# Kernel tuning notes

Hardware: AMD Instinct MI355X
Metric: run time of the kernel (lower is better)

The kernel has to match this reference:

```python
import jax, jax.numpy as jnp
import numpy as np

B, T = 64, 20          # batch, caption length
C, HW = 512, 196       # cnn_channels, width*height (14x14)
V, E, U = 10000, 256, 512  # n_tokens, emb_size, lstm_units
MAX_NORM = 5.0


def setup_inputs() -> dict:
    key = jax.random.key(0)
    ks = jax.random.split(key, 12)
    s = 0.02
    return {
        "image_features": jax.random.normal(ks[0], (B, C, HW), jnp.float32),
        "captions_ix": jax.random.randint(ks[1], (B, T), 0, V, dtype=jnp.int32),
        "W_h0": jax.random.normal(ks[2], (U, C), jnp.float32) * s,
        "b_h0": jnp.zeros((U,), jnp.float32),
        "W_c0": jax.random.normal(ks[3], (U, C), jnp.float32) * s,
        "b_c0": jnp.zeros((U,), jnp.float32),
        "emb": jax.random.normal(ks[4], (V, E), jnp.float32) * s,
        "W_key": jax.random.normal(ks[5], (U, C), jnp.float32) * s,
        "b_key": jnp.zeros((U,), jnp.float32),
        "W_ih": jax.random.normal(ks[6], (4 * U, C + E), jnp.float32) * s,
        "b_ih": jnp.zeros((4 * U,), jnp.float32),
        "W_hh": jax.random.normal(ks[7], (4 * U, U), jnp.float32) * s,
        "b_hh": jnp.zeros((4 * U,), jnp.float32),
        "W_out": jax.random.normal(ks[8], (V, C + E + U), jnp.float32) * s,
        "b_out": jnp.zeros((V,), jnp.float32),
    }


def _caption_net(image_features, captions_ix, W_h0, b_h0, W_c0, b_c0, emb,
                 W_key, b_key, W_ih, b_ih, W_hh, b_hh, W_out, b_out):
    feats_mean = image_features.mean(axis=2)                # [B, C]
    hid0 = feats_mean @ W_h0.T + b_h0                       # [B, U]
    cell0 = feats_mean @ W_c0.T + b_c0                      # [B, U]
    feats = jnp.transpose(image_features, (0, 2, 1))        # [B, HW, C]
    keys = feats @ W_key.T + b_key                          # [B, HW, U]

    # nn.Embedding(max_norm=5): renorm rows whose L2 norm exceeds 5
    norms = jnp.linalg.norm(emb, axis=1, keepdims=True)
    emb_eff = emb * jnp.minimum(1.0, MAX_NORM / jnp.maximum(norms, 1e-12))
    cap_emb = emb_eff[captions_ix]                          # [B, T, E]

    inv_scale = 1.0 / (keys.shape[2] ** 0.5)

    def step(carry, emb_t):
        hid, cell = carry
        # scaled dot-product attention, query = current hidden state
        scores = jnp.einsum('bu,bku->bk', hid, keys) * inv_scale   # [B, HW]
        w = jax.nn.softmax(scores, axis=1)
        a = jnp.einsum('bk,bkc->bc', w, feats)                     # [B, C]
        x = jnp.concatenate([emb_t, a], axis=1)                    # [B, E+C]
        gates = x @ W_ih.T + b_ih + hid @ W_hh.T + b_hh            # [B, 4U]
        i, f, g, o = jnp.split(gates, 4, axis=1)
        cell = jax.nn.sigmoid(f) * cell + jax.nn.sigmoid(i) * jnp.tanh(g)
        hid = jax.nn.sigmoid(o) * jnp.tanh(cell)
        out = jnp.concatenate([hid, a, emb_t], axis=1)             # [B, U+C+E]
        return (hid, cell), (out, w)

    (_, _), (outs, attn) = jax.lax.scan(step, (hid0, cell0),
                                        jnp.transpose(cap_emb, (1, 0, 2)))
    outs = jnp.transpose(outs, (1, 0, 2))                   # [B, T, U+C+E]
    attn = jnp.transpose(attn, (1, 0, 2))                   # [B, T, HW]
    logits = outs @ W_out.T + b_out                         # [B, T, V]
    return logits, attn


def reference(image_features, captions_ix, W_h0, b_h0, W_c0, b_c0, emb,
              W_key, b_key, W_ih, b_ih, W_hh, b_hh, W_out, b_out):
    return _caption_net(image_features, captions_ix, W_h0, b_h0, W_c0, b_c0,
                        emb, W_key, b_key, W_ih, b_ih, W_hh, b_hh, W_out, b_out)
```

## Files before the change

kernel.cpp:

```cpp
#include <hip/hip_runtime.h>
#include <math.h>

#define B 64
#define T 20
#define C 512
#define HW 196
#define V 10000
#define E 256
#define U 512
#define G4U 2048
#define ODIM 1280
#define KTOT 1280
#define NBLK 64

typedef short bf8_t __attribute__((ext_vector_type(8)));
typedef float f4_t  __attribute__((ext_vector_type(4)));

__device__ __forceinline__ unsigned short f2bf(float f) {
    unsigned int u = __float_as_uint(f);
    return (unsigned short)((u + 0x7fffu + ((u >> 16) & 1u)) >> 16);
}
__device__ __forceinline__ float bf2f(unsigned short s) {
    return __uint_as_float((unsigned int)s << 16);
}
__device__ __forceinline__ float bflo(unsigned int kv) { return __uint_as_float(kv << 16); }
__device__ __forceinline__ float bfhi(unsigned int kv) { return __uint_as_float(kv & 0xffff0000u); }

__device__ __forceinline__ void gbar(int* bar) {
    __syncthreads();
    if (threadIdx.x == 0) {
        __threadfence();
        int g = __hip_atomic_load(bar + 1, __ATOMIC_RELAXED, __HIP_MEMORY_SCOPE_AGENT);
        if (__hip_atomic_fetch_add(bar, 1, __ATOMIC_RELAXED, __HIP_MEMORY_SCOPE_AGENT) == NBLK - 1) {
            __hip_atomic_store(bar, 0, __ATOMIC_RELAXED, __HIP_MEMORY_SCOPE_AGENT);
            __hip_atomic_store(bar + 1, g + 1, __ATOMIC_RELEASE, __HIP_MEMORY_SCOPE_AGENT);
        } else {
            while (__hip_atomic_load(bar + 1, __ATOMIC_RELAXED, __HIP_MEMORY_SCOPE_AGENT) == g)
                __builtin_amdgcn_s_sleep(1);
        }
        __threadfence();
    }
    __syncthreads();
}

__global__ void k_mean(const float* __restrict__ img, float* __restrict__ fm,
                       int* __restrict__ bar) {
    if (blockIdx.x == 0 && threadIdx.x == 0) { bar[0] = 0; bar[1] = 0; }
    int wave = threadIdx.x >> 6;
    int lane = threadIdx.x & 63;
    int row = blockIdx.x * 4 + wave;
    const float* p = img + (size_t)row * HW;
    float s = p[lane] + p[lane + 64] + p[lane + 128];
    if (lane < 4) s += p[lane + 192];
    for (int off = 32; off > 0; off >>= 1) s += __shfl_down(s, off, 64);
    if (lane == 0) fm[row] = s * (1.0f / HW);
}

__global__ void k_init(const float* __restrict__ fm,
                       const float* __restrict__ W_h0, const float* __restrict__ b_h0,
                       const float* __restrict__ W_c0, const float* __restrict__ b_c0,
                       unsigned short* __restrict__ xb, float* __restrict__ cell) {
    int wv = blockIdx.x * 4 + (threadIdx.x >> 6);
    int lane = threadIdx.x & 63;
    int which = wv >> 15;
    int r = wv & 32767;
    int b = r >> 9, u = r & 511;
    const float* W = which ? W_c0 : W_h0;
    const float* bias = which ? b_c0 : b_h0;
    const float* f = fm + b * C;
    const float* w = W + (size_t)u * C;
    float s = 0.f;
    #pragma unroll
    for (int c = 0; c < C; c += 64) s += f[c + lane] * w[c + lane];
    for (int off = 32; off > 0; off >>= 1) s += __shfl_down(s, off, 64);
    if (lane == 0) {
        float v = s + bias[u];
        if (which) cell[r] = v;
        else       xb[(size_t)b * KTOT + 768 + u] = f2bf(v);
    }
}

__global__ void k_wkt(const float* __restrict__ Wk, float* __restrict__ WkT) {
    __shared__ float tile[64][65];
    int u0 = blockIdx.x * 64, c0 = blockIdx.y * 64;
    int x = threadIdx.x & 63, y0 = threadIdx.x >> 6;
    #pragma unroll
    for (int i = 0; i < 16; i++) {
        int r = y0 * 16 + i;
        tile[r][x] = Wk[(size_t)(u0 + r) * C + c0 + x];
    }
    __syncthreads();
    #pragma unroll
    for (int i = 0; i < 16; i++) {
        int r = y0 * 16 + i;
        WkT[(size_t)(c0 + r) * U + u0 + x] = tile[x][r];
    }
}

__global__ __launch_bounds__(256) void k_keys(const float* __restrict__ img,
        const float* __restrict__ WkT, const float* __restrict__ b_key,
        unsigned short* __restrict__ keys2) {
    __shared__ unsigned short st[32][200];
    int b = blockIdx.x >> 4;
    int u0 = (blockIdx.x & 15) * 32;
    int wave = __builtin_amdgcn_readfirstlane(threadIdx.x >> 6);
    int lane = threadIdx.x & 63;
    int lk = lane < 49 ? lane : 48;
    const f4_t* imgb = (const f4_t*)(img + (size_t)b * C * HW);
    f4_t acc[8];
    #pragma unroll
    for (int j = 0; j < 8; j++) acc[j] = (f4_t){0.f, 0.f, 0.f, 0.f};
    const float* wp = WkT + u0 + wave * 8;
    for (int c = 0; c < C; c++) {
        f4_t v = imgb[c * 49 + lk];
        const float* w = wp + (size_t)c * U;
        #pragma unroll
        for (int j = 0; j < 8; j++) acc[j] += v * w[j];
    }
    if (lane < 49) {
        #pragma unroll
        for (int j = 0; j < 8; j++) {
            float bk = b_key[u0 + wave * 8 + j];
            int ul = wave * 8 + j;
            int k = lane * 4;
            st[ul][k + 0] = f2bf(acc[j].x + bk);
            st[ul][k + 1] = f2bf(acc[j].y + bk);
            st[ul][k + 2] = f2bf(acc[j].z + bk);
            st[ul][k + 3] = f2bf(acc[j].w + bk);
        }
    }
    __syncthreads();
    int ui = threadIdx.x & 15;
    int kr = threadIdx.x >> 4;
    #pragma unroll
    for (int pass = 0; pass < 13; pass++) {
        int k = pass * 16 + kr;
        if (k < HW) {
            unsigned int lo = st[ui * 2][k];
            unsigned int hi = st[ui * 2 + 1][k];
            *(unsigned int*)&keys2[((size_t)b * HW + k) * U + u0 + ui * 2] = (hi << 16) | lo;
        }
    }
}

__global__ void k_wg(const float* __restrict__ W_ih, const float* __restrict__ W_hh,
                     unsigned short* __restrict__ Wg) {
    int j = blockIdx.x;
    int tid = threadIdx.x;
    const float* s1 = W_ih + (size_t)j * 768;
    const float* s2 = W_hh + (size_t)j * 512;
    unsigned short* dst = Wg + (size_t)j * KTOT;
    #pragma unroll
    for (int p = 0; p < 3; p++) dst[tid + p * 256] = f2bf(s1[tid + p * 256]);
    #pragma unroll
    for (int p = 0; p < 2; p++) dst[768 + tid + p * 256] = f2bf(s2[tid + p * 256]);
}

__global__ void k_emb(const int* __restrict__ ix, const float* __restrict__ emb,
                      unsigned short* __restrict__ outs) {
    int bt = blockIdx.x;
    int e = threadIdx.x;
    int row = ix[bt];
    float v = emb[(size_t)row * E + e];
    __shared__ float red[4];
    float sq = v * v;
    for (int off = 32; off > 0; off >>= 1) sq += __shfl_down(sq, off, 64);
    int wave = e >> 6, lane = e & 63;
    if (lane == 0) red[wave] = sq;
    __syncthreads();
    float norm = sqrtf(red[0] + red[1] + red[2] + red[3]);
    float scale = fminf(1.0f, 5.0f / fmaxf(norm, 1e-12f));
    outs[(size_t)bt * ODIM + (U + C) + e] = f2bf(v * scale);
}

__global__ __launch_bounds__(256) void k_wo(const float* __restrict__ W,
                                            unsigned short* __restrict__ Wb) {
    size_t i = ((size_t)blockIdx.x * 256 + threadIdx.x) * 8;
    float4 f0 = *(const float4*)(W + i);
    float4 f1 = *(const float4*)(W + i + 4);
    uint4 q;
    q.x = ((unsigned int)f2bf(f0.y) << 16) | f2bf(f0.x);
    q.y = ((unsigned int)f2bf(f0.w) << 16) | f2bf(f0.z);
    q.z = ((unsigned int)f2bf(f1.y) << 16) | f2bf(f1.x);
    q.w = ((unsigned int)f2bf(f1.w) << 16) | f2bf(f1.z);
    *(uint4*)(Wb + i) = q;
}

__global__ __launch_bounds__(256) void k_loop(
    unsigned short* __restrict__ outs, unsigned short* __restrict__ xb,
    const float* __restrict__ cell0, float* __restrict__ gates_buf,
    const unsigned short* __restrict__ keys2, const float* __restrict__ img,
    const float* __restrict__ b_ih, const float* __restrict__ b_hh,
    const unsigned short* __restrict__ Wg, float* __restrict__ attn,
    int* __restrict__ bar) {
    int b = blockIdx.x;
    int tid = threadIdx.x;
    int wave = __builtin_amdgcn_readfirstlane(tid >> 6);
    int lane = tid & 63;
    int m16 = lane & 15, quad = lane >> 4;
    __shared__ float hidS[U];
    __shared__ float wS[256];
    __shared__ float red[4];
    __shared__ unsigned short As2[64][72];
    __shared__ unsigned short Bs2[32][72];

    float c_r[2], bsum[2][4];
    #pragma unroll
    for (int p = 0; p < 2; p++) {
        int u = tid + p * 256;
        c_r[p] = cell0[(size_t)b * U + u];
        #pragma unroll
        for (int q = 0; q < 4; q++)
            bsum[p][q] = b_ih[q * 512 + u] + b_hh[q * 512 + u];
    }

    int j0g = blockIdx.x * 32;
    int r = tid >> 2, kq = tid & 3;
    int rb = tid >> 3, kb = tid & 7;
    int n16 = wave & 1, mpair = wave >> 1;

    for (int t = 0; t <= T; ++t) {
        if (t > 0) {
            #pragma unroll
            for (int p = 0; p < 2; p++) {
                int u = tid + p * 256;
                float g[4];
                #pragma unroll
                for (int q = 0; q < 4; q++)
                    g[q] = gates_buf[(size_t)b * G4U + q * 512 + u] + bsum[p][q];
                float si = 1.f / (1.f + expf(-g[0]));
                float sf = 1.f / (1.f + expf(-g[1]));
                float tg = tanhf(g[2]);
                float so = 1.f / (1.f + expf(-g[3]));
                float cn = sf * c_r[p] + si * tg;
                c_r[p] = cn;
                float hn = so * tanhf(cn);
                hidS[u] = hn;
                outs[((size_t)b * T + (t - 1)) * ODIM + u] = f2bf(hn);
                xb[(size_t)b * KTOT + 768 + u] = f2bf(hn);
            }
        } else {
            #pragma unroll
            for (int p = 0; p < 2; p++) {
                int u = tid + p * 256;
                hidS[u] = bf2f(xb[(size_t)b * KTOT + 768 + u]);
            }
        }
        if (t == T) break;
        __syncthreads();

        float sc = 0.f;
        if (tid < HW) {
            const uint4* kr = (const uint4*)(keys2 + ((size_t)b * HW + tid) * U);
            float acc = 0.f;
            #pragma unroll 8
            for (int i = 0; i < 64; i++) {
                uint4 kv = kr[i];
                float4 h0 = *(const float4*)&hidS[i * 8];
                float4 h1 = *(const float4*)&hidS[i * 8 + 4];
                acc += bflo(kv.x) * h0.x + bfhi(kv.x) * h0.y
                     + bflo(kv.y) * h0.z + bfhi(kv.y) * h0.w
                     + bflo(kv.z) * h1.x + bfhi(kv.z) * h1.y
                     + bflo(kv.w) * h1.z + bfhi(kv.w) * h1.w;
            }
            sc = acc * 0.044194173824159216f;
        }
        {
            float v = (tid < HW) ? sc : -1e30f;
            float m = v;
            for (int off = 32; off > 0; off >>= 1) m = fmaxf(m, __shfl_down(m, off, 64));
            if (lane == 0) red[wave] = m;
            __syncthreads();
            m = fmaxf(fmaxf(red[0], red[1]), fmaxf(red[2], red[3]));
            float ex = (tid < HW) ? expf(v - m) : 0.f;
            float ssum = ex;
            for (int off = 32; off > 0; off >>= 1) ssum += __shfl_down(ssum, off, 64);
            __syncthreads();
            if (lane == 0) red[wave] = ssum;
            __syncthreads();
            ssum = red[0] + red[1] + red[2] + red[3];
            float w = ex / ssum;
            wS[tid] = w;
            if (tid < HW) attn[((size_t)b * T + t) * HW + tid] = w;
        }
        __syncthreads();

        {
            const float4* imgb = (const float4*)(img + (size_t)b * C * HW);
            #pragma unroll
            for (int p = 0; p < 2; p++) {
                int c = tid + p * 256;
                const float4* rr4 = imgb + c * 49;
                float acc = 0.f;
                for (int k4 = 0; k4 < 49; k4++) {
                    float4 vv = rr4[k4];
                    acc += wS[4 * k4] * vv.x + wS[4 * k4 + 1] * vv.y
                         + wS[4 * k4 + 2] * vv.z + wS[4 * k4 + 3] * vv.w;
                }
                xb[(size_t)b * KTOT + 256 + c] = f2bf(acc);
                outs[((size_t)b * T + t) * ODIM + U + c] = f2bf(acc);
            }
        }
        if (tid < 128) {
            const unsigned int* src = (const unsigned int*)(outs + ((size_t)b * T + t) * ODIM);
            unsigned int* dst = (unsigned int*)(xb + (size_t)b * KTOT);
            dst[tid] = src[512 + tid];
        }

        gbar(bar);

        {
            f4_t acc2[2];
            acc2[0] = (f4_t){0.f, 0.f, 0.f, 0.f};
            acc2[1] = (f4_t){0.f, 0.f, 0.f, 0.f};
            const uint4* ap0 = (const uint4*)&xb[(size_t)r * KTOT + kq * 16];
            uint4 a0 = ap0[0], a1 = ap0[1];
            uint4 bq = *(const uint4*)&Wg[(size_t)(j0g + rb) * KTOT + kb * 8];
            for (int k0 = 0; k0 < KTOT; k0 += 64) {
                *(uint4*)&As2[r][kq * 16]     = a0;
                *(uint4*)&As2[r][kq * 16 + 8] = a1;
                *(uint4*)&Bs2[rb][kb * 8]     = bq;
                __syncthreads();
                if (k0 + 64 < KTOT) {
                    const uint4* apn = (const uint4*)&xb[(size_t)r * KTOT + k0 + 64 + kq * 16];
                    a0 = apn[0]; a1 = apn[1];
                    bq = *(const uint4*)&Wg[(size_t)(j0g + rb) * KTOT + k0 + 64 + kb * 8];
                }
                #pragma unroll
                for (int h = 0; h < 2; h++) {
                    bf8_t bfr = *(const bf8_t*)&Bs2[n16 * 16 + m16][h * 32 + quad * 8];
                    #pragma unroll
                    for (int i2 = 0; i2 < 2; i2++) {
                        bf8_t afr = *(const bf8_t*)&As2[(mpair * 2 + i2) * 16 + m16][h * 32 + quad * 8];
                        acc2[i2] = __builtin_amdgcn_mfma_f32_16x16x32_bf16(afr, bfr, acc2[i2], 0, 0, 0);
                    }
                }
                __syncthreads();
            }
            int n = j0g + n16 * 16 + m16;
            #pragma unroll
            for (int i2 = 0; i2 < 2; i2++) {
                int mb = (mpair * 2 + i2) * 16 + quad * 4;
                #pragma unroll
                for (int rr = 0; rr < 4; rr++)
                    gates_buf[(size_t)(mb + rr) * G4U + n] = acc2[i2][rr];
            }
        }

        gbar(bar);
    }
}

__global__ __launch_bounds__(256) void k_logits4(
    const unsigned short* __restrict__ A, const float* __restrict__ Wo,
    const float* __restrict__ bo, float* __restrict__ Cout) {
    __shared__ unsigned short As[128][72];
    __shared__ unsigned short Bs[128][72];
    int n0 = blockIdx.x * 128;
    int m0 = blockIdx.y * 128;
    int tid = threadIdx.x;
    int lane = tid & 63, wv = tid >> 6;
    int mw = (wv >> 1) * 64, nw = (wv & 1) * 64;
    int m16 = lane & 15, quad = lane >> 4;
    int srow = tid >> 1, shalf = tid & 1;

    f4_t acc[4][4];
    #pragma unroll
    for (int i = 0; i < 4; i++)
        #pragma unroll
        for (int j = 0; j < 4; j++)
            acc[i][j] = (f4_t){0.f, 0.f, 0.f, 0.f};

    for (int k0 = 0; k0 < KTOT; k0 += 64) {
        {
            const uint4* ap = (const uint4*)&A[(size_t)(m0 + srow) * KTOT + k0 + shalf * 32];
            uint4 a0 = ap[0], a1 = ap[1], a2 = ap[2], a3 = ap[3];
            uint4* dst = (uint4*)&As[srow][shalf * 32];
            dst[0] = a0; dst[1] = a1; dst[2] = a2; dst[3] = a3;
        }
        {
            int n = n0 + srow;
            uint4 q[4];
            if (n < V) {
                const float4* bp = (const float4*)&Wo[(size_t)n * KTOT + k0 + shalf * 32];
                #pragma unroll
                for (int g = 0; g < 4; g++) {
                    float4 f0 = bp[g * 2], f1 = bp[g * 2 + 1];
                    q[g].x = ((unsigned int)f2bf(f0.y) << 16) | f2bf(f0.x);
                    q[g].y = ((unsigned int)f2bf(f0.w) << 16) | f2bf(f0.z);
                    q[g].z = ((unsigned int)f2bf(f1.y) << 16) | f2bf(f1.x);
                    q[g].w = ((unsigned int)f2bf(f1.w) << 16) | f2bf(f1.z);
                }
            } else {
                #pragma unroll
                for (int g = 0; g < 4; g++) q[g] = (uint4){0u, 0u, 0u, 0u};
            }
            uint4* dst = (uint4*)&Bs[srow][shalf * 32];
            #pragma unroll
            for (int g = 0; g < 4; g++) dst[g] = q[g];
        }
        __syncthreads();
        #pragma unroll
        for (int h = 0; h < 2; h++) {
            bf8_t af[4], bf[4];
            #pragma unroll
            for (int i = 0; i < 4; i++)
                af[i] = *(const bf8_t*)&As[mw + i * 16 + m16][h * 32 + quad * 8];
            #pragma unroll
            for (int j = 0; j < 4; j++)
                bf[j] = *(const bf8_t*)&Bs[nw + j * 16 + m16][h * 32 + quad * 8];
            #pragma unroll
            for (int i = 0; i < 4; i++)
                #pragma unroll
                for (int j = 0; j < 4; j++)
                    acc[i][j] = __builtin_amdgcn_mfma_f32_16x16x32_bf16(af[i], bf[j], acc[i][j], 0, 0, 0);
        }
        __syncthreads();
    }

    #pragma unroll
    for (int j = 0; j < 4; j++) {
        int n = n0 + nw + j * 16 + m16;
        if (n >= V) continue;
        float bias = bo[n];
        #pragma unroll
        for (int i = 0; i < 4; i++) {
            int mb = m0 + mw + i * 16 + quad * 4;
            #pragma unroll
            for (int r = 0; r < 4; r++)
                Cout[(size_t)(mb + r) * V + n] = acc[i][j][r] + bias;
        }
    }
}

__global__ __launch_bounds__(256) void k_logits5(
    const unsigned short* __restrict__ A, const unsigned short* __restrict__ Wob,
    const float* __restrict__ bo, float* __restrict__ Cout) {
    __shared__ unsigned short As[128][72];
    __shared__ unsigned short Bs[128][72];
    int n0 = blockIdx.x * 128;
    int m0 = blockIdx.y * 128;
    int tid = threadIdx.x;
    int lane = tid & 63, wv = tid >> 6;
    int mw = (wv >> 1) * 64, nw = (wv & 1) * 64;
    int m16 = lane & 15, quad = lane >> 4;
    int srow = tid >> 1, shalf = tid & 1;

    f4_t acc[4][4];
    #pragma unroll
    for (int i = 0; i < 4; i++)
        #pragma unroll
        for (int j = 0; j < 4; j++)
            acc[i][j] = (f4_t){0.f, 0.f, 0.f, 0.f};

    for (int k0 = 0; k0 < KTOT; k0 += 64) {
        {
            const uint4* ap = (const uint4*)&A[(size_t)(m0 + srow) * KTOT + k0 + shalf * 32];
            uint4 a0 = ap[0], a1 = ap[1], a2 = ap[2], a3 = ap[3];
            uint4* dst = (uint4*)&As[srow][shalf * 32];
            dst[0] = a0; dst[1] = a1; dst[2] = a2; dst[3] = a3;
        }
        {
            int n = n0 + srow;
            uint4 q[4];
            if (n < V) {
                const uint4* bp = (const uint4*)&Wob[(size_t)n * KTOT + k0 + shalf * 32];
                #pragma unroll
                for (int g = 0; g < 4; g++) q[g] = bp[g];
            } else {
                #pragma unroll
                for (int g = 0; g < 4; g++) q[g] = (uint4){0u, 0u, 0u, 0u};
            }
            uint4* dst = (uint4*)&Bs[srow][shalf * 32];
            #pragma unroll
            for (int g = 0; g < 4; g++) dst[g] = q[g];
        }
        __syncthreads();
        #pragma unroll
        for (int h = 0; h < 2; h++) {
            bf8_t af[4], bf[4];
            #pragma unroll
            for (int i = 0; i < 4; i++)
                af[i] = *(const bf8_t*)&As[mw + i * 16 + m16][h * 32 + quad * 8];
            #pragma unroll
            for (int j = 0; j < 4; j++)
                bf[j] = *(const bf8_t*)&Bs[nw + j * 16 + m16][h * 32 + quad * 8];
            #pragma unroll
            for (int i = 0; i < 4; i++)
                #pragma unroll
                for (int j = 0; j < 4; j++)
                    acc[i][j] = __builtin_amdgcn_mfma_f32_16x16x32_bf16(af[i], bf[j], acc[i][j], 0, 0, 0);
        }
        __syncthreads();
    }

    #pragma unroll
    for (int j = 0; j < 4; j++) {
        int n = n0 + nw + j * 16 + m16;
        if (n >= V) continue;
        float bias = bo[n];
        #pragma unroll
        for (int i = 0; i < 4; i++) {
            int mb = m0 + mw + i * 16 + quad * 4;
            #pragma unroll
            for (int r = 0; r < 4; r++)
                Cout[(size_t)(mb + r) * V + n] = acc[i][j][r] + bias;
        }
    }
}

extern "C" void kernel_launch(void* const* d_in, const int* in_sizes, int n_in,
                              void* d_out, int out_size, void* d_ws, size_t ws_size,
                              hipStream_t stream) {
    const float* img   = (const float*)d_in[0];
    const int*   capix = (const int*)d_in[1];
    const float* W_h0  = (const float*)d_in[2];
    const float* b_h0  = (const float*)d_in[3];
    const float* W_c0  = (const float*)d_in[4];
    const float* b_c0  = (const float*)d_in[5];
    const float* emb   = (const float*)d_in[6];
    const float* W_key = (const float*)d_in[7];
    const float* b_key = (const float*)d_in[8];
    const float* W_ih  = (const float*)d_in[9];
    const float* b_ih  = (const float*)d_in[10];
    const float* W_hh  = (const float*)d_in[11];
    const float* b_hh  = (const float*)d_in[12];
    const float* W_out = (const float*)d_in[13];
    const float* b_out = (const float*)d_in[14];

    float* ws = (float*)d_ws;
    float* gates_buf = ws;
    float* fm        = ws;
    float* cell      = gates_buf + 131072;
    float* WkT       = cell + 32768;
    unsigned short* Wg    = (unsigned short*)(WkT + 262144);
    unsigned short* xb    = Wg + 2621440;
    unsigned short* outs  = xb + 81920;
    unsigned short* keys2 = outs + (size_t)B * T * ODIM;
    int* bar = (int*)(keys2 + (size_t)B * HW * U);
    const size_t WOB_OFF = 23232576;
    unsigned short* Wob = (unsigned short*)((char*)d_ws + WOB_OFF);
    bool use_wob = ws_size >= WOB_OFF + (size_t)V * KTOT * 2;

    float* logits = (float*)d_out;
    float* attn   = logits + (size_t)B * T * V;

    k_mean<<<(B * C) / 4, 256, 0, stream>>>(img, fm, bar);
    k_init<<<(2 * B * U) / 4, 256, 0, stream>>>(fm, W_h0, b_h0, W_c0, b_c0, xb, cell);
    k_wkt<<<dim3(8, 8), 256, 0, stream>>>(W_key, WkT);
    k_keys<<<B * 16, 256, 0, stream>>>(img, WkT, b_key, keys2);
    k_wg<<<G4U, 256, 0, stream>>>(W_ih, W_hh, Wg);
    k_emb<<<B * T, 256, 0, stream>>>(capix, emb, outs);
    if (use_wob)
        k_wo<<<(V * KTOT) / 2048, 256, 0, stream>>>(W_out, Wob);

    k_loop<<<NBLK, 256, 0, stream>>>(outs, xb, cell, gates_buf, keys2, img,
                                     b_ih, b_hh, Wg, attn, bar);

    if (use_wob)
        k_logits5<<<dim3((V + 127) / 128, (B * T) / 128), 256, 0, stream>>>(outs, Wob, b_out, logits);
    else
        k_logits4<<<dim3((V + 127) / 128, (B * T) / 128), 256, 0, stream>>>(outs, W_out, b_out, logits);
}
```

Baseline: 1.438 ms.

## Replace grid-barrier threadfences with cache-bypassing loads/stores and interleave gate layout

Removes the __threadfence calls from the software grid barrier. Cross-block data (xb, gates) is now written and read with sc0 sc1 global loads and stores, which bypass the non-coherent caches, so ordering relies on vmcnt waits instead of full fences. The gates buffer is relaid out as [b][u][4] so each thread fetches its four gate values with one vector load. This targets the per-step barrier cost of the recurrent loop, at the risk of subtle memory-ordering bugs if the cache-bypass assumption does not hold on this hardware.

```diff
diff --git a/kernel.cpp b/kernel.cpp
--- a/kernel.cpp
+++ b/kernel.cpp
@@ -26,10 +26,35 @@
 __device__ __forceinline__ float bflo(unsigned int kv) { return __uint_as_float(kv << 16); }
 __device__ __forceinline__ float bfhi(unsigned int kv) { return __uint_as_float(kv & 0xffff0000u); }
 
+__device__ __forceinline__ void coh_load4x2(const void* p0, const void* p1,
+                                            uint4& r0, uint4& r1) {
+    asm volatile("global_load_dwordx4 %0, %2, off sc0 sc1\n\t"
+                 "global_load_dwordx4 %1, %3, off sc0 sc1\n\t"
+                 "s_waitcnt vmcnt(0)"
+                 : "=&v"(r0), "=&v"(r1) : "v"(p0), "v"(p1) : "memory");
+}
+__device__ __forceinline__ void coh_load4_issue(const void* p, uint4& r) {
+    asm volatile("global_load_dwordx4 %0, %1, off sc0 sc1"
+                 : "=&v"(r) : "v"(p) : "memory");
+}
+__device__ __forceinline__ void wait_vm0() {
+    asm volatile("s_waitcnt vmcnt(0)" ::: "memory");
+    __builtin_amdgcn_sched_barrier(0);
+}
+__device__ __forceinline__ void coh_store1f(void* p, float v) {
+    asm volatile("global_store_dword %0, %1, off sc0 sc1" :: "v"(p), "v"(v) : "memory");
+}
+__device__ __forceinline__ void coh_store1u(void* p, unsigned int v) {
+    asm volatile("global_store_dword %0, %1, off sc0 sc1" :: "v"(p), "v"(v) : "memory");
+}
+__device__ __forceinline__ void coh_store_us(void* p, unsigned int v) {
+    asm volatile("global_store_short %0, %1, off sc0 sc1" :: "v"(p), "v"(v) : "memory");
+}
+
 __device__ __forceinline__ void gbar(int* bar) {
+    asm volatile("s_waitcnt vmcnt(0)" ::: "memory");
     __syncthreads();
     if (threadIdx.x == 0) {
-        __threadfence();
         int g = __hip_atomic_load(bar + 1, __ATOMIC_RELAXED, __HIP_MEMORY_SCOPE_AGENT);
         if (__hip_atomic_fetch_add(bar, 1, __ATOMIC_RELAXED, __HIP_MEMORY_SCOPE_AGENT) == NBLK - 1) {
             __hip_atomic_store(bar, 0, __ATOMIC_RELAXED, __HIP_MEMORY_SCOPE_AGENT);
@@ -38,7 +63,6 @@
             while (__hip_atomic_load(bar + 1, __ATOMIC_RELAXED, __HIP_MEMORY_SCOPE_AGENT) == g)
                 __builtin_amdgcn_s_sleep(1);
         }
-        __threadfence();
     }
     __syncthreads();
 }
@@ -188,7 +212,7 @@
 
 __global__ __launch_bounds__(256) void k_loop(
     unsigned short* __restrict__ outs, unsigned short* __restrict__ xb,
-    const float* __restrict__ cell0, float* __restrict__ gates_buf,
+    const float* __restrict__ cell0, float* __restrict__ gates4,
     const unsigned short* __restrict__ keys2, const float* __restrict__ img,
     const float* __restrict__ b_ih, const float* __restrict__ b_hh,
     const unsigned short* __restrict__ Wg, float* __restrict__ attn,
@@ -221,23 +245,28 @@
 
     for (int t = 0; t <= T; ++t) {
         if (t > 0) {
+            const float* g0 = gates4 + (size_t)b * 2048 + tid * 4;
+            uint4 r0, r1;
+            coh_load4x2(g0, g0 + 1024, r0, r1);
             #pragma unroll
             for (int p = 0; p < 2; p++) {
                 int u = tid + p * 256;
-                float g[4];
-                #pragma unroll
-                for (int q = 0; q < 4; q++)
-                    g[q] = gates_buf[(size_t)b * G4U + q * 512 + u] + bsum[p][q];
-                float si = 1.f / (1.f + expf(-g[0]));
-                float sf = 1.f / (1.f + expf(-g[1]));
-                float tg = tanhf(g[2]);
-                float so = 1.f / (1.f + expf(-g[3]));
+                float4 gv = p ? *(float4*)&r1 : *(float4*)&r0;
+                float g0f = gv.x + bsum[p][0];
+                float g1f = gv.y + bsum[p][1];
+                float g2f = gv.z + bsum[p][2];
+                float g3f = gv.w + bsum[p][3];
+                float si = 1.f / (1.f + expf(-g0f));
+                float sf = 1.f / (1.f + expf(-g1f));
+                float tg = tanhf(g2f);
+                float so = 1.f / (1.f + expf(-g3f));
                 float cn = sf * c_r[p] + si * tg;
                 c_r[p] = cn;
                 float hn = so * tanhf(cn);
                 hidS[u] = hn;
-                outs[((size_t)b * T + (t - 1)) * ODIM + u] = f2bf(hn);
-                xb[(size_t)b * KTOT + 768 + u] = f2bf(hn);
+                unsigned int hv = f2bf(hn);
+                outs[((size_t)b * T + (t - 1)) * ODIM + u] = (unsigned short)hv;
+                coh_store_us(&xb[(size_t)b * KTOT + 768 + u], hv);
             }
         } else {
             #pragma unroll
@@ -297,14 +326,15 @@
                     acc += wS[4 * k4] * vv.x + wS[4 * k4 + 1] * vv.y
                          + wS[4 * k4 + 2] * vv.z + wS[4 * k4 + 3] * vv.w;
                 }
-                xb[(size_t)b * KTOT + 256 + c] = f2bf(acc);
-                outs[((size_t)b * T + t) * ODIM + U + c] = f2bf(acc);
+                unsigned int av = f2bf(acc);
+                coh_store_us(&xb[(size_t)b * KTOT + 256 + c], av);
+                outs[((size_t)b * T + t) * ODIM + U + c] = (unsigned short)av;
             }
         }
         if (tid < 128) {
             const unsigned int* src = (const unsigned int*)(outs + ((size_t)b * T + t) * ODIM);
             unsigned int* dst = (unsigned int*)(xb + (size_t)b * KTOT);
-            dst[tid] = src[512 + tid];
+            coh_store1u(&dst[tid], src[512 + tid]);
         }
 
         gbar(bar);
@@ -313,18 +343,22 @@
             f4_t acc2[2];
             acc2[0] = (f4_t){0.f, 0.f, 0.f, 0.f};
             acc2[1] = (f4_t){0.f, 0.f, 0.f, 0.f};
-            const uint4* ap0 = (const uint4*)&xb[(size_t)r * KTOT + kq * 16];
-            uint4 a0 = ap0[0], a1 = ap0[1];
-            uint4 bq = *(const uint4*)&Wg[(size_t)(j0g + rb) * KTOT + kb * 8];
+            const unsigned short* xrow = xb + (size_t)r * KTOT + kq * 16;
+            const unsigned short* wrow = Wg + (size_t)(j0g + rb) * KTOT + kb * 8;
+            uint4 a0, a1, bq;
+            coh_load4x2(xrow, xrow + 8, a0, a1);
+            bq = *(const uint4*)wrow;
             for (int k0 = 0; k0 < KTOT; k0 += 64) {
                 *(uint4*)&As2[r][kq * 16]     = a0;
                 *(uint4*)&As2[r][kq * 16 + 8] = a1;
                 *(uint4*)&Bs2[rb][kb * 8]     = bq;
                 __syncthreads();
-                if (k0 + 64 < KTOT) {
-                    const uint4* apn = (const uint4*)&xb[(size_t)r * KTOT + k0 + 64 + kq * 16];
-                    a0 = apn[0]; a1 = apn[1];
-                    bq = *(const uint4*)&Wg[(size_t)(j0g + rb) * KTOT + k0 + 64 + kb * 8];
+                uint4 na0, na1, nbq;
+                bool more = (k0 + 64 < KTOT);
+                if (more) {
+                    coh_load4_issue(xrow + k0 + 64, na0);
+                    coh_load4_issue(xrow + k0 + 64 + 8, na1);
+                    nbq = *(const uint4*)(wrow + k0 + 64);
                 }
                 #pragma unroll
                 for (int h = 0; h < 2; h++) {
@@ -335,15 +369,21 @@
                         acc2[i2] = __builtin_amdgcn_mfma_f32_16x16x32_bf16(afr, bfr, acc2[i2], 0, 0, 0);
                     }
                 }
+                if (more) {
+                    wait_vm0();
+                    a0 = na0; a1 = na1; bq = nbq;
+                }
                 __syncthreads();
             }
             int n = j0g + n16 * 16 + m16;
+            int qq = n >> 9, uu = n & 511;
+            float* gbase = gates4 + (size_t)uu * 4 + qq;
             #pragma unroll
             for (int i2 = 0; i2 < 2; i2++) {
                 int mb = (mpair * 2 + i2) * 16 + quad * 4;
                 #pragma unroll
                 for (int rr = 0; rr < 4; rr++)
-                    gates_buf[(size_t)(mb + rr) * G4U + n] = acc2[i2][rr];
+                    coh_store1f(gbase + (size_t)(mb + rr) * 2048, acc2[i2][rr]);
             }
         }
 
@@ -529,9 +569,9 @@
     const float* b_out = (const float*)d_in[14];
 
     float* ws = (float*)d_ws;
-    float* gates_buf = ws;
+    float* gates4    = ws;
     float* fm        = ws;
-    float* cell      = gates_buf + 131072;
+    float* cell      = gates4 + 131072;
     float* WkT       = cell + 32768;
     unsigned short* Wg    = (unsigned short*)(WkT + 262144);
     unsigned short* xb    = Wg + 2621440;
@@ -554,7 +594,7 @@
     if (use_wob)
         k_wo<<<(V * KTOT) / 2048, 256, 0, stream>>>(W_out, Wob);
 
-    k_loop<<<NBLK, 256, 0, stream>>>(outs, xb, cell, gates_buf, keys2, img,
+    k_loop<<<NBLK, 256, 0, stream>>>(outs, xb, cell, gates4, keys2, img,
                                      b_ih, b_hh, Wg, attn, bar);
 
     if (use_wob)
```

New measurement: 1.230 ms. 14.4% less time.
